# Performance work log

Measured on AMD Instinct MI355X. Metric: run time of the kernel, lower is better.

## Reference

```python
import jax, jax.numpy as jnp
import numpy as np

B, C, H, W = 16, 256, 64, 64


def _conv1x1(x, w, b):
    # x: [B,C,H,W], w: [O,C], b: [O]
    return jnp.einsum('oc,bchw->bohw', w, x) + b[None, :, None, None]


def _maxpool2(x):
    b, c, h, w = x.shape
    return x.reshape(b, c, h // 2, 2, w // 2, 2).max(axis=(3, 5))


def setup_inputs() -> dict:
    key = jax.random.key(0)
    ks = jax.random.split(key, 10)
    c8, c2 = C // 8, C // 2
    s = lambda fan_in: 1.0 / np.sqrt(fan_in)
    return {
        'x': jax.random.normal(ks[0], (B, C, H, W), dtype=jnp.float32),
        'query_w': jax.random.normal(ks[1], (c8, C), dtype=jnp.float32) * s(C),
        'query_b': jnp.zeros((c8,), dtype=jnp.float32),
        'key_w': jax.random.normal(ks[2], (c8, C), dtype=jnp.float32) * s(C),
        'key_b': jnp.zeros((c8,), dtype=jnp.float32),
        'val_w': jax.random.normal(ks[3], (c2, C), dtype=jnp.float32) * s(C),
        'val_b': jnp.zeros((c2,), dtype=jnp.float32),
        'val2_w': jax.random.normal(ks[4], (C, c2), dtype=jnp.float32) * s(c2),
        'val2_b': jnp.zeros((C,), dtype=jnp.float32),
        'gamma': jnp.zeros((1,), dtype=jnp.float32) + 0.5,  # nonzero so attention path contributes
    }


def reference(x, query_w, query_b, key_w, key_b, val_w, val_b, val2_w, val2_b, gamma):
    b, nc, h, w = x.shape
    loc = h * w
    down = loc // 4
    c8, c2 = nc // 8, nc // 2

    # query: conv then raw view to [B, HW, C//8] (NOT a permute; faithful to torch .view)
    q = _conv1x1(x, query_w, query_b)              # [B, C/8, H, W]
    q = q.reshape(b, loc, c8)                      # raw reshape, mixes channel/spatial

    # key: conv -> 2x2 maxpool -> raw view -> permute(0,2,1)
    k = _maxpool2(_conv1x1(x, key_w, key_b))       # [B, C/8, H/2, W/2]
    k = k.reshape(b, down, c8).transpose(0, 2, 1)  # [B, C/8, down]

    # value: conv -> 2x2 maxpool -> raw view
    v = _maxpool2(_conv1x1(x, val_w, val_b))       # [B, C/2, H/2, W/2]
    v = v.reshape(b, down, c2)                     # [B, down, C/2]

    attn = jnp.einsum('bqd,bdk->bqk', q, k)        # [B, HW, down], no 1/sqrt(d)
    attn_weights = jax.nn.softmax(attn, axis=1)    # softmax over QUERY axis (dim=1), as in source
    applied = jnp.einsum('bqk,bkc->bqc', attn_weights, v)  # [B, HW, C/2]

    # raw view back to [B, C/2, w, h] (note w,h swapped in source)
    applied = applied.reshape(b, c2, w, h)
    out = _conv1x1(applied, val2_w, val2_b)        # [B, C, w, h]
    return gamma * out + x
```

## Files before the change

### kernel.cpp

```cpp
#include <hip/hip_runtime.h>
#include <hip/hip_bf16.h>


typedef short s8v __attribute__((ext_vector_type(8)));
typedef float f4v __attribute__((ext_vector_type(4)));
typedef unsigned short u16v8 __attribute__((ext_vector_type(8)));

#define MFMA16(a, b, c) __builtin_amdgcn_mfma_f32_16x16x32_bf16((a), (b), (c), 0, 0, 0)
#define LOG2E 1.4426950408889634f

__device__ __forceinline__ unsigned short f2b(float f) {
    __hip_bfloat16 h = __float2bfloat16(f);
    return *reinterpret_cast<unsigned short*>(&h);
}
__device__ __forceinline__ float b2f(unsigned short u) {
    union { unsigned int i; float f; } v; v.i = ((unsigned int)u) << 16; return v.f;
}
__device__ __forceinline__ void async_lds16(const void* g, void* l) {
    __builtin_amdgcn_global_load_lds(
        (const __attribute__((address_space(1))) void*)g,
        (__attribute__((address_space(3))) void*)l, 16, 0, 0);
}

__global__ void prep_weights(const float* __restrict__ qw, const float* __restrict__ qb,
                             const float* __restrict__ kw, const float* __restrict__ kb,
                             const float* __restrict__ vw, const float* __restrict__ vb,
                             const float* __restrict__ v2w,
                             unsigned short* __restrict__ wqkv, float* __restrict__ bias,
                             unsigned short* __restrict__ w2b) {
    int i = blockIdx.x * 256 + threadIdx.x;
    if (i < 49152) {
        int r = i >> 8, c = i & 255; float v;
        if (r < 32)       v = qw[r * 256 + c];
        else if (r < 64)  v = kw[(r - 32) * 256 + c] * LOG2E;
        else              v = vw[(r - 64) * 256 + c];
        wqkv[i] = f2b(v);
    } else if (i < 49152 + 32768) {
        int k = i - 49152; w2b[k] = f2b(v2w[k]);
    } else if (i < 49152 + 32768 + 192) {
        int r = i - 49152 - 32768;
        bias[r] = (r < 32) ? qb[r] : (r < 64 ? kb[r - 32] * LOG2E : vb[r - 64]);
    }
}

template <typename T>
__global__ __launch_bounds__(256) void transpose_v8(const T* __restrict__ src,
                                                    unsigned short* __restrict__ dst,
                                                    int R, int C) {
    __shared__ float tile[64][65];
    int b = blockIdx.z;
    size_t base = (size_t)b * R * C;
    int r0 = blockIdx.x * 64, c0 = blockIdx.y * 64;
    int rl = threadIdx.x >> 3;
    int g  = threadIdx.x & 7;
    #pragma unroll
    for (int rr = 0; rr < 2; ++rr) {
        int r = rr * 32 + rl;
        const T* p = src + base + (size_t)(r0 + r) * C + c0 + g * 8;
        if constexpr (sizeof(T) == 4) {
            float4 a = *(const float4*)p;
            float4 bq = *(const float4*)(p + 4);
            tile[r][g * 8 + 0] = a.x;  tile[r][g * 8 + 1] = a.y;
            tile[r][g * 8 + 2] = a.z;  tile[r][g * 8 + 3] = a.w;
            tile[r][g * 8 + 4] = bq.x; tile[r][g * 8 + 5] = bq.y;
            tile[r][g * 8 + 6] = bq.z; tile[r][g * 8 + 7] = bq.w;
        } else {
            u16v8 a = *(const u16v8*)p;
            #pragma unroll
            for (int i = 0; i < 8; ++i) tile[r][g * 8 + i] = b2f((unsigned short)a[i]);
        }
    }
    __syncthreads();
    #pragma unroll
    for (int rr = 0; rr < 2; ++rr) {
        int c = rr * 32 + rl;
        u16v8 o;
        #pragma unroll
        for (int i = 0; i < 8; ++i) o[i] = f2b(tile[g * 8 + i][c]);
        *(u16v8*)(dst + base + (size_t)(c0 + c) * R + r0 + g * 8) = o;
    }
}

__global__ __launch_bounds__(256) void transpose_scale_v(const unsigned short* __restrict__ src,
                                                         const float* __restrict__ rs,
                                                         unsigned short* __restrict__ dst) {
    __shared__ float tile[64][65];
    int b = blockIdx.z;
    size_t base = (size_t)b * 131072;
    int r0 = blockIdx.x * 64, c0 = blockIdx.y * 64;
    int tr = threadIdx.x >> 6, tc = threadIdx.x & 63;
    float scale = rs[b * 1024 + r0 + tc];
    for (int i = 0; i < 16; ++i) {
        int rl = i * 4 + tr;
        tile[rl][tc] = b2f(src[base + (size_t)(r0 + rl) * 128 + c0 + tc]);
    }
    __syncthreads();
    for (int i = 0; i < 16; ++i) {
        int cl = i * 4 + tr;
        int c = c0 + cl;
        int j = r0 + tc;
        int jc = j >> 7, jl = j & 127, g = jl >> 3, e = jl & 7;
        dst[base + jc * 16384 + c * 128 + ((g ^ (c & 7)) << 3) + e] =
            f2b(tile[tc][cl] * scale);
    }
}

__global__ __launch_bounds__(256) void qkv_pool(const unsigned short* __restrict__ wqkv,
                                                const float* __restrict__ bias,
                                                const unsigned short* __restrict__ xbt,
                                                unsigned short* __restrict__ qf,
                                                unsigned short* __restrict__ kf,
                                                unsigned short* __restrict__ vf) {
    int b = blockIdx.y, r = blockIdx.x;
    int p0 = r * 128;
    int wave = threadIdx.x >> 6, lane = threadIdx.x & 63;
    int m = lane & 15, quad = lane >> 4;
    const unsigned short* xb = xbt + (size_t)b * 4096 * 256;

    f4v acc[3][8] = {};
    for (int ks = 0; ks < 8; ++ks) {
        int k0 = ks * 32 + quad * 8;
        s8v afr[3];
        for (int mt = 0; mt < 3; ++mt)
            afr[mt] = *(const s8v*)(wqkv + (wave * 48 + mt * 16 + m) * 256 + k0);
        for (int nt = 0; nt < 8; ++nt) {
            s8v bfr = *(const s8v*)(xb + (size_t)(p0 + nt * 16 + m) * 256 + k0);
            for (int mt = 0; mt < 3; ++mt)
                acc[mt][nt] = MFMA16(afr[mt], bfr, acc[mt][nt]);
        }
    }
    for (int mt = 0; mt < 3; ++mt) {
        int obase = wave * 48 + mt * 16;
        if (obase < 32) {
            for (int reg = 0; reg < 4; ++reg) {
                int o = obase + quad * 4 + reg;
                float bi = bias[o];
                for (int nt = 0; nt < 8; ++nt)
                    qf[(size_t)b * 131072 + (size_t)o * 4096 + p0 + nt * 16 + m] =
                        f2b(acc[mt][nt][reg] + bi);
            }
        } else {
            for (int reg = 0; reg < 4; ++reg) {
                int o = obase + quad * 4 + reg;
                float bi = bias[o];
                for (int nt = 0; nt < 4; ++nt) {
                    float vv = fmaxf(acc[mt][nt][reg], acc[mt][nt + 4][reg]);
                    float ov = __shfl_xor(vv, 1);
                    if ((m & 1) == 0) {
                        float res = fmaxf(vv, ov) + bi;
                        int w2 = nt * 8 + (m >> 1);
                        int sp = r * 32 + w2;
                        if (o < 64) kf[(size_t)b * 32768 + (size_t)(o - 32) * 1024 + sp] = f2b(res);
                        else        vf[(size_t)b * 131072 + (size_t)(o - 64) * 1024 + sp] = f2b(res);
                    }
                }
            }
        }
    }
}

__global__ __launch_bounds__(256) void col_stats(const unsigned short* __restrict__ qf,
                                                 const unsigned short* __restrict__ kf,
                                                 float* __restrict__ rs) {
    __shared__ float red[4][16];
    int b = blockIdx.y, j0 = blockIdx.x * 16;
    int wave = threadIdx.x >> 6, lane = threadIdx.x & 63;
    int m = lane & 15, quad = lane >> 4;
    const unsigned short* qb = qf + (size_t)b * 131072;
    f4v zero = {0.f, 0.f, 0.f, 0.f};

    s8v kfr = *(const s8v*)(kf + (size_t)b * 32768 + (size_t)(j0 + m) * 32 + quad * 8);

    float sm = 0.f;
    for (int it = wave; it < 256; it += 4) {
        s8v afr = *(const s8v*)(qb + (size_t)(it * 16 + m) * 32 + quad * 8);
        f4v s = MFMA16(afr, kfr, zero);
        sm += (exp2f(s[0]) + exp2f(s[1])) + (exp2f(s[2]) + exp2f(s[3]));
    }
    sm += __shfl_xor(sm, 16);
    sm += __shfl_xor(sm, 32);
    if (lane < 16) red[wave][m] = sm;
    __syncthreads();
    if (threadIdx.x < 16) {
        float S = (red[0][threadIdx.x] + red[1][threadIdx.x]) +
                  (red[2][threadIdx.x] + red[3][threadIdx.x]);
        rs[b * 1024 + j0 + threadIdx.x] = 1.0f / S;
    }
}

__global__ __launch_bounds__(512, 4) void attn_fused(const unsigned short* __restrict__ qf,
                                                     const unsigned short* __restrict__ kf,
                                                     const unsigned short* __restrict__ vsw,
                                                     unsigned short* __restrict__ fa) {
    __shared__ alignas(16) unsigned short VS[16384];
    __shared__ alignas(16) unsigned short PT[16384];
    int b = blockIdx.y, l0 = blockIdx.x * 128;
    int tid = threadIdx.x;
    int wave = tid >> 6, lane = tid & 63;
    int m = lane & 15, quad = lane >> 4;
    int ls = wave * 16;
    const unsigned short* qb = qf + (size_t)b * 131072;
    const unsigned short* kb = kf + (size_t)b * 32768;
    const unsigned short* vb = vsw + (size_t)b * 131072;

    s8v qa = *(const s8v*)(qb + (size_t)(l0 + ls + m) * 32 + quad * 8);
    f4v acc[8] = {};
    f4v zero = {0.f, 0.f, 0.f, 0.f};

    for (int jc = 0; jc < 8; ++jc) {
        {
            const unsigned short* src = vb + jc * 16384 + tid * 8;
            unsigned short* dstl = VS + tid * 8;
            for (int rnd = 0; rnd < 4; ++rnd)
                async_lds16(src + rnd * 4096, dstl + rnd * 4096);
        }
        int j0 = jc * 128;
        int l = ls + m;
        for (int jt = 0; jt < 8; ++jt) {
            s8v kfr = *(const s8v*)(kb + (size_t)(j0 + jt * 16 + m) * 32 + quad * 8);
            f4v st = MFMA16(kfr, qa, zero);
            unsigned int u0 = ((unsigned)f2b(exp2f(st[1])) << 16) |
                              (unsigned)f2b(exp2f(st[0]));
            unsigned int u1 = ((unsigned)f2b(exp2f(st[3])) << 16) |
                              (unsigned)f2b(exp2f(st[2]));
            int g = jt * 2 + (quad >> 1);
            int sub = (quad & 1) * 4;
            uint2 uu; uu.x = u0; uu.y = u1;
            *(uint2*)(&PT[l * 128 + ((g ^ (l & 7)) << 3) + sub]) = uu;
        }
        __syncthreads();
        __builtin_amdgcn_s_setprio(1);
        for (int ks = 0; ks < 4; ++ks) {
            int gp = ks * 4 + quad;
            s8v pa = *(const s8v*)(&PT[l * 128 + ((gp ^ (l & 7)) << 3)]);
            for (int ct = 0; ct < 8; ++ct) {
                int c = ct * 16 + m;
                s8v vfr = *(const s8v*)(&VS[c * 128 + ((gp ^ (c & 7)) << 3)]);
                acc[ct] = MFMA16(pa, vfr, acc[ct]);
            }
        }
        __builtin_amdgcn_s_setprio(0);
        __syncthreads();
    }
    for (int ct = 0; ct < 8; ++ct)
        for (int reg = 0; reg < 4; ++reg) {
            int l = l0 + ls + quad * 4 + reg;
            fa[(size_t)b * 524288 + (size_t)l * 128 + ct * 16 + m] = f2b(acc[ct][reg]);
        }
}

__global__ __launch_bounds__(256, 4) void final_gemm(const unsigned short* __restrict__ w2b,
                                                     const float* __restrict__ v2b,
                                                     const float* __restrict__ gamma,
                                                     const unsigned short* __restrict__ ga,
                                                     const float* __restrict__ x,
                                                     float* __restrict__ out) {
    int b = blockIdx.z, p0 = blockIdx.x * 64;
    int wave = threadIdx.x >> 6, lane = threadIdx.x & 63;
    int m = lane & 15, quad = lane >> 4;
    int obase = blockIdx.y * 128 + wave * 32;
    const unsigned short* gb = ga + (size_t)b * 524288;

    float4 xv[2][4];
    #pragma unroll
    for (int mt = 0; mt < 2; ++mt) {
        size_t xrow = (size_t)b * 1048576 + (size_t)(obase + mt * 16 + m) * 4096;
        #pragma unroll
        for (int nt = 0; nt < 4; ++nt)
            xv[mt][nt] = *(const float4*)(x + xrow + p0 + nt * 16 + quad * 4);
    }

    f4v acc[2][4] = {};
    for (int ks = 0; ks < 4; ++ks) {
        int k0 = ks * 32 + quad * 8;
        s8v afr[2], bfr[4];
        #pragma unroll
        for (int mt = 0; mt < 2; ++mt)
            afr[mt] = *(const s8v*)(w2b + (obase + mt * 16 + m) * 128 + k0);
        #pragma unroll
        for (int nt = 0; nt < 4; ++nt)
            bfr[nt] = *(const s8v*)(gb + (size_t)(p0 + nt * 16 + m) * 128 + k0);
        #pragma unroll
        for (int mt = 0; mt < 2; ++mt)
            #pragma unroll
            for (int nt = 0; nt < 4; ++nt)
                acc[mt][nt] = MFMA16(bfr[nt], afr[mt], acc[mt][nt]);
    }
    float g = gamma[0];
    #pragma unroll
    for (int mt = 0; mt < 2; ++mt) {
        int o = obase + mt * 16 + m;
        float bi = v2b[o];
        size_t xrow = (size_t)b * 1048576 + (size_t)o * 4096;
        #pragma unroll
        for (int nt = 0; nt < 4; ++nt) {
            size_t xi = xrow + p0 + nt * 16 + quad * 4;
            float4 ov;
            ov.x = g * (acc[mt][nt][0] + bi) + xv[mt][nt].x;
            ov.y = g * (acc[mt][nt][1] + bi) + xv[mt][nt].y;
            ov.z = g * (acc[mt][nt][2] + bi) + xv[mt][nt].z;
            ov.w = g * (acc[mt][nt][3] + bi) + xv[mt][nt].w;
            *(float4*)(out + xi) = ov;
        }
    }
}

extern "C" void kernel_launch(void* const* d_in, const int* in_sizes, int n_in,
                              void* d_out, int out_size, void* d_ws, size_t ws_size,
                              hipStream_t stream) {
    const float* x    = (const float*)d_in[0];
    const float* qw   = (const float*)d_in[1];
    const float* qb   = (const float*)d_in[2];
    const float* kw   = (const float*)d_in[3];
    const float* kb   = (const float*)d_in[4];
    const float* vw   = (const float*)d_in[5];
    const float* vb   = (const float*)d_in[6];
    const float* v2w  = (const float*)d_in[7];
    const float* v2b  = (const float*)d_in[8];
    const float* gamma = (const float*)d_in[9];
    float* out = (float*)d_out;

    char* ws = (char*)d_ws;
    size_t off = 0;
    auto alloc = [&](size_t bytes) { size_t o = off; off = (off + bytes + 255) & ~(size_t)255; return o; };
    unsigned short* wqkv = (unsigned short*)(ws + alloc(192 * 256 * 2));
    unsigned short* w2b  = (unsigned short*)(ws + alloc(256 * 128 * 2));
    float*          bias = (float*)(ws + alloc(192 * 4));
    float*          rs   = (float*)(ws + alloc((size_t)16 * 1024 * 4));
    unsigned short* qf   = (unsigned short*)(ws + alloc((size_t)16 * 131072 * 2));
    unsigned short* kf   = (unsigned short*)(ws + alloc((size_t)16 * 32768 * 2));
    unsigned short* vf   = (unsigned short*)(ws + alloc((size_t)16 * 131072 * 2));
    unsigned short* vt   = (unsigned short*)(ws + alloc((size_t)16 * 131072 * 2));
    unsigned short* fa   = (unsigned short*)(ws + alloc((size_t)16 * 524288 * 2));
    char*           big  = ws + alloc((size_t)16 * 4096 * 256 * 2);
    unsigned short* xbt  = (unsigned short*)big;
    unsigned short* ga   = (unsigned short*)big;
    (void)ws_size; (void)in_sizes; (void)n_in; (void)out_size;

    prep_weights<<<321, 256, 0, stream>>>(qw, qb, kw, kb, vw, vb, v2w, wqkv, bias, w2b);
    transpose_v8<float><<<dim3(4, 64, 16), 256, 0, stream>>>(x, xbt, 256, 4096);
    qkv_pool<<<dim3(32, 16), 256, 0, stream>>>(wqkv, bias, xbt, qf, kf, vf);
    col_stats<<<dim3(64, 16), 256, 0, stream>>>(qf, kf, rs);
    transpose_scale_v<<<dim3(16, 2, 16), 256, 0, stream>>>(vf, rs, vt);
    attn_fused<<<dim3(32, 16), 512, 0, stream>>>(qf, kf, vt, fa);
    transpose_v8<unsigned short><<<dim3(2, 64, 16), 256, 0, stream>>>(fa, ga, 128, 4096);
    final_gemm<<<dim3(64, 2, 16), 256, 0, stream>>>(w2b, v2b, gamma, ga, x, out);
}
```

Baseline: 268.1 us.

## Fuse weight prep into x transpose, fold fa transpose into final GEMM, shrink attention blocks

```diff
diff --git a/kernel.cpp b/kernel.cpp
--- a/kernel.cpp
+++ b/kernel.cpp
@@ -22,62 +22,57 @@
         (__attribute__((address_space(3))) void*)l, 16, 0, 0);
 }
 
-__global__ void prep_weights(const float* __restrict__ qw, const float* __restrict__ qb,
-                             const float* __restrict__ kw, const float* __restrict__ kb,
-                             const float* __restrict__ vw, const float* __restrict__ vb,
-                             const float* __restrict__ v2w,
-                             unsigned short* __restrict__ wqkv, float* __restrict__ bias,
-                             unsigned short* __restrict__ w2b) {
-    int i = blockIdx.x * 256 + threadIdx.x;
-    if (i < 49152) {
-        int r = i >> 8, c = i & 255; float v;
-        if (r < 32)       v = qw[r * 256 + c];
-        else if (r < 64)  v = kw[(r - 32) * 256 + c] * LOG2E;
-        else              v = vw[(r - 64) * 256 + c];
-        wqkv[i] = f2b(v);
-    } else if (i < 49152 + 32768) {
-        int k = i - 49152; w2b[k] = f2b(v2w[k]);
-    } else if (i < 49152 + 32768 + 192) {
-        int r = i - 49152 - 32768;
-        bias[r] = (r < 32) ? qb[r] : (r < 64 ? kb[r - 32] * LOG2E : vb[r - 64]);
-    }
-}
-
-template <typename T>
-__global__ __launch_bounds__(256) void transpose_v8(const T* __restrict__ src,
-                                                    unsigned short* __restrict__ dst,
-                                                    int R, int C) {
-    __shared__ float tile[64][65];
-    int b = blockIdx.z;
-    size_t base = (size_t)b * R * C;
-    int r0 = blockIdx.x * 64, c0 = blockIdx.y * 64;
-    int rl = threadIdx.x >> 3;
-    int g  = threadIdx.x & 7;
-    #pragma unroll
-    for (int rr = 0; rr < 2; ++rr) {
-        int r = rr * 32 + rl;
-        const T* p = src + base + (size_t)(r0 + r) * C + c0 + g * 8;
-        if constexpr (sizeof(T) == 4) {
+__global__ __launch_bounds__(256) void prologue(const float* __restrict__ x,
+                                                unsigned short* __restrict__ xbt,
+                                                const float* __restrict__ qw, const float* __restrict__ qb,
+                                                const float* __restrict__ kw, const float* __restrict__ kb,
+                                                const float* __restrict__ vw, const float* __restrict__ vb,
+                                                const float* __restrict__ v2w,
+                                                unsigned short* __restrict__ wqkv,
+                                                float* __restrict__ bias,
+                                                unsigned short* __restrict__ w2b) {
+    int bid = blockIdx.x;
+    if (bid < 4096) {
+        __shared__ float tile[64][65];
+        int bx = bid & 3, by = (bid >> 2) & 63, bz = bid >> 8;
+        size_t base = (size_t)bz * 1048576;
+        int r0 = bx * 64, c0 = by * 64;
+        int rl = threadIdx.x >> 3;
+        int g  = threadIdx.x & 7;
+        #pragma unroll
+        for (int rr = 0; rr < 2; ++rr) {
+            int r = rr * 32 + rl;
+            const float* p = x + base + (size_t)(r0 + r) * 4096 + c0 + g * 8;
             float4 a = *(const float4*)p;
             float4 bq = *(const float4*)(p + 4);
             tile[r][g * 8 + 0] = a.x;  tile[r][g * 8 + 1] = a.y;
             tile[r][g * 8 + 2] = a.z;  tile[r][g * 8 + 3] = a.w;
             tile[r][g * 8 + 4] = bq.x; tile[r][g * 8 + 5] = bq.y;
             tile[r][g * 8 + 6] = bq.z; tile[r][g * 8 + 7] = bq.w;
-        } else {
-            u16v8 a = *(const u16v8*)p;
+        }
+        __syncthreads();
+        #pragma unroll
+        for (int rr = 0; rr < 2; ++rr) {
+            int c = rr * 32 + rl;
+            u16v8 o;
             #pragma unroll
-            for (int i = 0; i < 8; ++i) tile[r][g * 8 + i] = b2f((unsigned short)a[i]);
-        }
-    }
-    __syncthreads();
-    #pragma unroll
-    for (int rr = 0; rr < 2; ++rr) {
-        int c = rr * 32 + rl;
-        u16v8 o;
-        #pragma unroll
-        for (int i = 0; i < 8; ++i) o[i] = f2b(tile[g * 8 + i][c]);
-        *(u16v8*)(dst + base + (size_t)(c0 + c) * R + r0 + g * 8) = o;
+            for (int i = 0; i < 8; ++i) o[i] = f2b(tile[g * 8 + i][c]);
+            *(u16v8*)(xbt + base + (size_t)(c0 + c) * 256 + r0 + g * 8) = o;
+        }
+    } else {
+        int i = (bid - 4096) * 256 + threadIdx.x;
+        if (i < 49152) {
+            int r = i >> 8, c = i & 255; float v;
+            if (r < 32)       v = qw[r * 256 + c];
+            else if (r < 64)  v = kw[(r - 32) * 256 + c] * LOG2E;
+            else              v = vw[(r - 64) * 256 + c];
+            wqkv[i] = f2b(v);
+        } else if (i < 49152 + 32768) {
+            int k = i - 49152; w2b[k] = f2b(v2w[k]);
+        } else if (i < 49152 + 32768 + 192) {
+            int r = i - 49152 - 32768;
+            bias[r] = (r < 32) ? qb[r] : (r < 64 ? kb[r - 32] * LOG2E : vb[r - 64]);
+        }
     }
 }
 
@@ -188,13 +183,13 @@
     }
 }
 
-__global__ __launch_bounds__(512, 4) void attn_fused(const unsigned short* __restrict__ qf,
+__global__ __launch_bounds__(256, 3) void attn_fused(const unsigned short* __restrict__ qf,
                                                      const unsigned short* __restrict__ kf,
                                                      const unsigned short* __restrict__ vsw,
                                                      unsigned short* __restrict__ fa) {
     __shared__ alignas(16) unsigned short VS[16384];
-    __shared__ alignas(16) unsigned short PT[16384];
-    int b = blockIdx.y, l0 = blockIdx.x * 128;
+    __shared__ alignas(16) unsigned short PT[8192];
+    int b = blockIdx.y, l0 = blockIdx.x * 64;
     int tid = threadIdx.x;
     int wave = tid >> 6, lane = tid & 63;
     int m = lane & 15, quad = lane >> 4;
@@ -211,8 +206,8 @@
         {
             const unsigned short* src = vb + jc * 16384 + tid * 8;
             unsigned short* dstl = VS + tid * 8;
-            for (int rnd = 0; rnd < 4; ++rnd)
-                async_lds16(src + rnd * 4096, dstl + rnd * 4096);
+            for (int rnd = 0; rnd < 8; ++rnd)
+                async_lds16(src + rnd * 2048, dstl + rnd * 2048);
         }
         int j0 = jc * 128;
         int l = ls + m;
@@ -252,14 +247,26 @@
 __global__ __launch_bounds__(256, 4) void final_gemm(const unsigned short* __restrict__ w2b,
                                                      const float* __restrict__ v2b,
                                                      const float* __restrict__ gamma,
-                                                     const unsigned short* __restrict__ ga,
+                                                     const unsigned short* __restrict__ fa,
                                                      const float* __restrict__ x,
                                                      float* __restrict__ out) {
-    int b = blockIdx.z, p0 = blockIdx.x * 64;
+    __shared__ alignas(16) unsigned short gt[64][136];
+    int b = blockIdx.z, bx = blockIdx.x;
+    int p0 = bx * 64;
+    int page = bx >> 1;
+    int c0 = (bx & 1) * 64;
     int wave = threadIdx.x >> 6, lane = threadIdx.x & 63;
     int m = lane & 15, quad = lane >> 4;
     int obase = blockIdx.y * 128 + wave * 32;
-    const unsigned short* gb = ga + (size_t)b * 524288;
+
+    int row  = threadIdx.x >> 1;
+    int half = threadIdx.x & 1;
+    const unsigned short* fr = fa + (size_t)b * 524288 +
+                               (size_t)(row * 32 + page) * 128 + c0 + half * 32;
+    u16v8 t0 = *(const u16v8*)(fr);
+    u16v8 t1 = *(const u16v8*)(fr + 8);
+    u16v8 t2 = *(const u16v8*)(fr + 16);
+    u16v8 t3 = *(const u16v8*)(fr + 24);
 
     float4 xv[2][4];
     #pragma unroll
@@ -270,6 +277,18 @@
             xv[mt][nt] = *(const float4*)(x + xrow + p0 + nt * 16 + quad * 4);
     }
 
+    {
+        int pb = half * 32;
+        #pragma unroll
+        for (int i = 0; i < 8; ++i) {
+            gt[pb + i][row]      = t0[i];
+            gt[pb + 8 + i][row]  = t1[i];
+            gt[pb + 16 + i][row] = t2[i];
+            gt[pb + 24 + i][row] = t3[i];
+        }
+    }
+    __syncthreads();
+
     f4v acc[2][4] = {};
     for (int ks = 0; ks < 4; ++ks) {
         int k0 = ks * 32 + quad * 8;
@@ -279,7 +298,7 @@
             afr[mt] = *(const s8v*)(w2b + (obase + mt * 16 + m) * 128 + k0);
         #pragma unroll
         for (int nt = 0; nt < 4; ++nt)
-            bfr[nt] = *(const s8v*)(gb + (size_t)(p0 + nt * 16 + m) * 128 + k0);
+            bfr[nt] = *(const s8v*)(&gt[nt * 16 + m][k0]);
         #pragma unroll
         for (int mt = 0; mt < 2; ++mt)
             #pragma unroll
@@ -332,17 +351,13 @@
     unsigned short* vf   = (unsigned short*)(ws + alloc((size_t)16 * 131072 * 2));
     unsigned short* vt   = (unsigned short*)(ws + alloc((size_t)16 * 131072 * 2));
     unsigned short* fa   = (unsigned short*)(ws + alloc((size_t)16 * 524288 * 2));
-    char*           big  = ws + alloc((size_t)16 * 4096 * 256 * 2);
-    unsigned short* xbt  = (unsigned short*)big;
-    unsigned short* ga   = (unsigned short*)big;
+    unsigned short* xbt  = (unsigned short*)(ws + alloc((size_t)16 * 4096 * 256 * 2));
     (void)ws_size; (void)in_sizes; (void)n_in; (void)out_size;
 
-    prep_weights<<<321, 256, 0, stream>>>(qw, qb, kw, kb, vw, vb, v2w, wqkv, bias, w2b);
-    transpose_v8<float><<<dim3(4, 64, 16), 256, 0, stream>>>(x, xbt, 256, 4096);
+    prologue<<<4417, 256, 0, stream>>>(x, xbt, qw, qb, kw, kb, vw, vb, v2w, wqkv, bias, w2b);
     qkv_pool<<<dim3(32, 16), 256, 0, stream>>>(wqkv, bias, xbt, qf, kf, vf);
     col_stats<<<dim3(64, 16), 256, 0, stream>>>(qf, kf, rs);
     transpose_scale_v<<<dim3(16, 2, 16), 256, 0, stream>>>(vf, rs, vt);
-    attn_fused<<<dim3(32, 16), 512, 0, stream>>>(qf, kf, vt, fa);
-    transpose_v8<unsigned short><<<dim3(2, 64, 16), 256, 0, stream>>>(fa, ga, 128, 4096);
-    final_gemm<<<dim3(64, 2, 16), 256, 0, stream>>>(w2b, v2b, gamma, ga, x, out);
-}
+    attn_fused<<<dim3(64, 16), 256, 0, stream>>>(qf, kf, vt, fa);
+    final_gemm<<<dim3(64, 2, 16), 256, 0, stream>>>(w2b, v2b, gamma, fa, x, out);
+}
```

Measured after the change: 259.9 us. 3.0% less time.
